# Optimization experiments

Measured on AMD Instinct MI355X. Metric: run time of the kernel, lower is better.

The kernel has to match this reference:

```python
import jax, jax.numpy as jnp
import numpy as np

N_NODES = 8192
N_EDGES = 262144
IN_DIM = 128
HID = 256


def _sage_conv(x, src, dst, w_l, b_l, w_r, n):
    # PyG SAGEConv: out = lin_l(mean_{j in N(i)} x_j) + lin_r(x_i)
    agg = jax.ops.segment_sum(x[src], dst, num_segments=n)          # [n, d]
    deg = jax.ops.segment_sum(jnp.ones_like(src, dtype=x.dtype), dst, num_segments=n)
    mean = agg / jnp.maximum(deg, 1.0)[:, None]
    return mean @ w_l.T + b_l + x @ w_r.T


def setup_inputs() -> dict:
    key = jax.random.key(0)
    ks = jax.random.split(key, 12)
    s = lambda d: 1.0 / np.sqrt(d)
    x = jax.random.normal(ks[0], (N_NODES, IN_DIM), dtype=jnp.float32)
    edge_index = jax.random.randint(ks[1], (2, N_EDGES), 0, N_NODES, dtype=jnp.int64)
    return {
        "x": x,
        "edge_index": edge_index,
        "wl1": jax.random.uniform(ks[2], (HID, IN_DIM), jnp.float32, -s(IN_DIM), s(IN_DIM)),
        "bl1": jax.random.uniform(ks[3], (HID,), jnp.float32, -s(IN_DIM), s(IN_DIM)),
        "wr1": jax.random.uniform(ks[4], (HID, IN_DIM), jnp.float32, -s(IN_DIM), s(IN_DIM)),
        "wl2": jax.random.uniform(ks[5], (HID, HID), jnp.float32, -s(HID), s(HID)),
        "bl2": jax.random.uniform(ks[6], (HID,), jnp.float32, -s(HID), s(HID)),
        "wr2": jax.random.uniform(ks[7], (HID, HID), jnp.float32, -s(HID), s(HID)),
        "w_out": jax.random.uniform(ks[8], (HID, HID), jnp.float32, -s(HID), s(HID)),
        "b_out": jax.random.uniform(ks[9], (HID,), jnp.float32, -s(HID), s(HID)),
        "w_edge": jax.random.uniform(ks[10], (1, 2 * HID), jnp.float32, -s(2 * HID), s(2 * HID)),
        "b_edge": jax.random.uniform(ks[11], (1,), jnp.float32, -s(2 * HID), s(2 * HID)),
    }


def reference(x, edge_index, wl1, bl1, wr1, wl2, bl2, wr2, w_out, b_out, w_edge, b_edge):
    n = x.shape[0]
    src, dst = edge_index[0], edge_index[1]
    h = jax.nn.relu(_sage_conv(x, src, dst, wl1, bl1, wr1, n))
    h = jax.nn.relu(_sage_conv(h, src, dst, wl2, bl2, wr2, n))
    h = h @ w_out.T + b_out                                          # [n, HID]
    # edge_logits[i, j] = edge_proj(cat(h_i, h_j)) == <w_left, h_i> + <w_right, h_j> + b
    w_left, w_right = w_edge[0, :HID], w_edge[0, HID:]
    li = h @ w_left                                                  # [n]
    lj = h @ w_right                                                 # [n]
    return li[:, None] + lj[None, :] + b_edge[0]                     # [n, n]
```

## Files before the change

kernel.cpp:

```cpp
#include <hip/hip_runtime.h>

#define NN   8192
#define NE   262144
#define IND  128
#define HIDD 256

typedef __bf16 v8bf __attribute__((ext_vector_type(8)));
typedef float  v4f  __attribute__((ext_vector_type(4)));

__device__ __forceinline__ float bf2f(unsigned short u) {
  unsigned int v = ((unsigned int)u) << 16;
  return __builtin_bit_cast(float, v);
}
__device__ __forceinline__ unsigned short f2bf(float f) {
  unsigned int u = __builtin_bit_cast(unsigned int, f);
  u += 0x7FFF + ((u >> 16) & 1);
  return (unsigned short)(u >> 16);
}

__global__ void k_prep(const float* __restrict__ wl1, const float* __restrict__ wr1,
                       const float* __restrict__ wl2, const float* __restrict__ wr2,
                       const float* __restrict__ x,
                       const float* __restrict__ w_out, const float* __restrict__ b_out,
                       const float* __restrict__ w_edge,
                       unsigned short* __restrict__ W1, unsigned short* __restrict__ W2,
                       unsigned short* __restrict__ A1,
                       float* __restrict__ VL, float* __restrict__ VR,
                       float* __restrict__ C2,
                       int* __restrict__ CNT,
                       float* __restrict__ LI, float* __restrict__ LJ) {
  __shared__ float red[256];
  int b = blockIdx.x, tid = threadIdx.x;
  if (b < 256) {
    int t = b * 256 + tid;
    int n = t >> 8, k = t & 255;
    float v = (k < 128) ? wl1[n * 128 + k] : wr1[n * 128 + (k - 128)];
    W1[t] = f2bf(v);
  } else if (b < 768) {
    int t = (b - 256) * 256 + tid;
    int n = t >> 9, k = t & 511;
    float v = (k < 256) ? wl2[n * 256 + k] : wr2[n * 256 + (k - 256)];
    W2[t] = f2bf(v);
  } else if (b < 1280) {
    int t = (b - 768) * 256 + tid;
    int row = t >> 4, c8 = (t & 15) << 3;
    const float* xp = &x[row * 128 + c8];
    float4 a = *(const float4*)xp;
    float4 bb = *(const float4*)(xp + 4);
    unsigned short o[8];
    o[0] = f2bf(a.x);  o[1] = f2bf(a.y);  o[2] = f2bf(a.z);  o[3] = f2bf(a.w);
    o[4] = f2bf(bb.x); o[5] = f2bf(bb.y); o[6] = f2bf(bb.z); o[7] = f2bf(bb.w);
    *(uint4*)&A1[row * 256 + 128 + c8] = *(uint4*)o;
  } else if (b < 1312) {
    CNT[(b - 1280) * 256 + tid] = 0;
  } else if (b < 1344) {
    int t = (b - 1312) * 256 + tid;
    LI[t] = 0.f; LJ[t] = 0.f;
  } else {
    int k = tid;
    float al = 0.f, ar = 0.f;
    for (int n = 0; n < 256; n += 8) {
#pragma unroll
      for (int u = 0; u < 8; u++) {
        float w = w_out[(n + u) * 256 + k];
        al = fmaf(w, w_edge[n + u], al);
        ar = fmaf(w, w_edge[256 + n + u], ar);
      }
    }
    VL[k] = al; VR[k] = ar;
    red[k] = b_out[k] * w_edge[k];
    __syncthreads();
    for (int s = 128; s > 0; s >>= 1) { if (k < s) red[k] += red[k + s]; __syncthreads(); }
    if (k == 0) C2[0] = red[0];
    __syncthreads();
    red[k] = b_out[k] * w_edge[256 + k];
    __syncthreads();
    for (int s = 128; s > 0; s >>= 1) { if (k < s) red[k] += red[k + s]; __syncthreads(); }
    if (k == 0) C2[1] = red[0];
  }
}

__global__ void k_count(const int* __restrict__ dst, int* __restrict__ counts) {
  int e = blockIdx.x * 256 + threadIdx.x;
  if (e < NE) atomicAdd(&counts[dst[e]], 1);
}
__global__ void k_scan(const int* __restrict__ counts, int* __restrict__ offs,
                       int* __restrict__ curs, float* __restrict__ ideg) {
  __shared__ int sums[256];
  int t = threadIdx.x;
  int base = t * 32;
  int c[32];
#pragma unroll
  for (int i = 0; i < 32; i += 4) *(int4*)&c[i] = *(const int4*)&counts[base + i];
  int s = 0;
#pragma unroll
  for (int i = 0; i < 32; i++) s += c[i];
  sums[t] = s;
  __syncthreads();
  for (int off = 1; off < 256; off <<= 1) {
    int v = (t >= off) ? sums[t - off] : 0;
    __syncthreads();
    sums[t] += v;
    __syncthreads();
  }
  int run = (t == 0) ? 0 : sums[t - 1];
#pragma unroll
  for (int i = 0; i < 32; i++) {
    offs[base + i] = run;
    curs[base + i] = run;
    ideg[base + i] = 1.0f / (float)(c[i] > 0 ? c[i] : 1);
    run += c[i];
  }
}
__global__ void k_fill(const int* __restrict__ src, const int* __restrict__ dst,
                       int* __restrict__ curs, int* __restrict__ csr) {
  int e = blockIdx.x * 256 + threadIdx.x;
  if (e < NE) {
    int d = dst[e];
    int p = atomicAdd(&curs[d], 1);
    csr[p] = src[e];
  }
}

__global__ void k_gather1(const float* __restrict__ x, unsigned short* __restrict__ A1,
                          const int* __restrict__ offs, const int* __restrict__ counts,
                          const float* __restrict__ ideg, const int* __restrict__ csr) {
  int lane = threadIdx.x & 63;
  int node = blockIdx.x * 4 + (threadIdx.x >> 6);
  int start = offs[node], cnt = counts[node];
  const float2* fp = (const float2*)x + lane;
  float ax0 = 0.f, ay0 = 0.f, ax1 = 0.f, ay1 = 0.f;
  int i = 0;
  for (; i + 8 <= cnt; i += 8) {
    int s0 = csr[start + i + 0], s1 = csr[start + i + 1];
    int s2 = csr[start + i + 2], s3 = csr[start + i + 3];
    int s4 = csr[start + i + 4], s5 = csr[start + i + 5];
    int s6 = csr[start + i + 6], s7 = csr[start + i + 7];
    float2 v0 = fp[(size_t)s0 * 64], v1 = fp[(size_t)s1 * 64];
    float2 v2 = fp[(size_t)s2 * 64], v3 = fp[(size_t)s3 * 64];
    float2 v4 = fp[(size_t)s4 * 64], v5 = fp[(size_t)s5 * 64];
    float2 v6 = fp[(size_t)s6 * 64], v7 = fp[(size_t)s7 * 64];
    ax0 += v0.x; ay0 += v0.y; ax0 += v1.x; ay0 += v1.y;
    ax0 += v2.x; ay0 += v2.y; ax0 += v3.x; ay0 += v3.y;
    ax1 += v4.x; ay1 += v4.y; ax1 += v5.x; ay1 += v5.y;
    ax1 += v6.x; ay1 += v6.y; ax1 += v7.x; ay1 += v7.y;
  }
  for (; i < cnt; i++) {
    float2 v = fp[(size_t)csr[start + i] * 64];
    ax0 += v.x; ay0 += v.y;
  }
  float sc = ideg[node];
  float mx = (ax0 + ax1) * sc, my = (ay0 + ay1) * sc;
  unsigned int o = (unsigned int)f2bf(mx) | ((unsigned int)f2bf(my) << 16);
  *(unsigned int*)&A1[(size_t)node * 256 + lane * 2] = o;
}

__global__ void k_gather2(const unsigned short* __restrict__ A2,
                          unsigned short* __restrict__ A2w,
                          const int* __restrict__ offs, const int* __restrict__ counts,
                          const float* __restrict__ ideg, const int* __restrict__ csr) {
  int lane = threadIdx.x & 63;
  int node = blockIdx.x * 4 + (threadIdx.x >> 6);
  int start = offs[node], cnt = counts[node];
  const unsigned short* fp = A2 + 256 + lane * 4;
  float a0 = 0.f, a1 = 0.f, a2 = 0.f, a3 = 0.f;
#define ACC4(v) { a0 += bf2f((unsigned short)((v).x));        \
                  a1 += bf2f((unsigned short)((v).x >> 16));  \
                  a2 += bf2f((unsigned short)((v).y));        \
                  a3 += bf2f((unsigned short)((v).y >> 16)); }
  int i = 0;
  for (; i + 4 <= cnt; i += 4) {
    int s0 = csr[start + i + 0], s1 = csr[start + i + 1];
    int s2 = csr[start + i + 2], s3 = csr[start + i + 3];
    uint2 v0 = *(const uint2*)&fp[(size_t)s0 * 512];
    uint2 v1 = *(const uint2*)&fp[(size_t)s1 * 512];
    uint2 v2 = *(const uint2*)&fp[(size_t)s2 * 512];
    uint2 v3 = *(const uint2*)&fp[(size_t)s3 * 512];
    ACC4(v0); ACC4(v1); ACC4(v2); ACC4(v3);
  }
  for (; i < cnt; i++) {
    uint2 v = *(const uint2*)&fp[(size_t)csr[start + i] * 512];
    ACC4(v);
  }
#undef ACC4
  float sc = ideg[node];
  unsigned int lo = (unsigned int)f2bf(a0 * sc) | ((unsigned int)f2bf(a1 * sc) << 16);
  unsigned int hi = (unsigned int)f2bf(a2 * sc) | ((unsigned int)f2bf(a3 * sc) << 16);
  uint2 o; o.x = lo; o.y = hi;
  *(uint2*)&A2w[(size_t)node * 512 + lane * 4] = o;
}

__global__ __launch_bounds__(256) void k_gemm(
    const unsigned short* __restrict__ A, int lda,
    const unsigned short* __restrict__ B,
    const float* __restrict__ bias,
    unsigned short* __restrict__ C, int ldc, int coff, int K) {
  __shared__ __align__(16) unsigned short As[64][40];
  __shared__ __align__(16) unsigned short Bs[64][40];
  int tid = threadIdx.x;
  int bm = blockIdx.x, bn = blockIdx.y;
  int lane = tid & 63, wave = tid >> 6;
  int wm = (wave & 1) * 32, wn = (wave >> 1) * 32;
  int quad = lane >> 4, l16 = lane & 15;
  int srow = tid >> 2, schunk = (tid & 3) * 8;
  const unsigned short* gA = A + (size_t)(bm * 64 + srow) * lda + schunk;
  const unsigned short* gB = B + (size_t)(bn * 64 + srow) * K + schunk;
  v4f acc[2][2];
  for (int mi = 0; mi < 2; mi++)
    for (int ni = 0; ni < 2; ni++)
      acc[mi][ni] = v4f{0.f, 0.f, 0.f, 0.f};
  for (int k0 = 0; k0 < K; k0 += 32) {
    uint4 va = *(const uint4*)(gA + k0);
    uint4 vb = *(const uint4*)(gB + k0);
    __syncthreads();
    *(uint4*)&As[srow][schunk] = va;
    *(uint4*)&Bs[srow][schunk] = vb;
    __syncthreads();
    v8bf a0 = *(v8bf*)&As[wm + l16][quad * 8];
    v8bf a1 = *(v8bf*)&As[wm + 16 + l16][quad * 8];
    v8bf b0 = *(v8bf*)&Bs[wn + l16][quad * 8];
    v8bf b1 = *(v8bf*)&Bs[wn + 16 + l16][quad * 8];
    acc[0][0] = __builtin_amdgcn_mfma_f32_16x16x32_bf16(a0, b0, acc[0][0], 0, 0, 0);
    acc[0][1] = __builtin_amdgcn_mfma_f32_16x16x32_bf16(a0, b1, acc[0][1], 0, 0, 0);
    acc[1][0] = __builtin_amdgcn_mfma_f32_16x16x32_bf16(a1, b0, acc[1][0], 0, 0, 0);
    acc[1][1] = __builtin_amdgcn_mfma_f32_16x16x32_bf16(a1, b1, acc[1][1], 0, 0, 0);
  }
  for (int mi = 0; mi < 2; mi++) {
    for (int ni = 0; ni < 2; ni++) {
      int col = bn * 64 + wn + ni * 16 + l16;
      float bv = bias[col];
      for (int r = 0; r < 4; r++) {
        int row = bm * 64 + wm + mi * 16 + quad * 4 + r;
        float v = acc[mi][ni][r] + bv;
        v = fmaxf(v, 0.f);
        C[(size_t)row * ldc + coff + col] = f2bf(v);
      }
    }
  }
}

__global__ __launch_bounds__(256) void k_gemm2_lilj(
    const unsigned short* __restrict__ A,
    const unsigned short* __restrict__ B,
    const float* __restrict__ bias,
    const float* __restrict__ VL, const float* __restrict__ VR,
    float* __restrict__ LI, float* __restrict__ LJ) {
  __shared__ __align__(16) unsigned short As[64][40];
  __shared__ __align__(16) unsigned short Bs[64][40];
  int tid = threadIdx.x;
  int bm = blockIdx.x, bn = blockIdx.y;
  int lane = tid & 63, wave = tid >> 6;
  int wm = (wave & 1) * 32, wn = (wave >> 1) * 32;
  int quad = lane >> 4, l16 = lane & 15;
  int srow = tid >> 2, schunk = (tid & 3) * 8;
  const unsigned short* gA = A + (size_t)(bm * 64 + srow) * 512 + schunk;
  const unsigned short* gB = B + (size_t)(bn * 64 + srow) * 512 + schunk;
  v4f acc[2][2];
  for (int mi = 0; mi < 2; mi++)
    for (int ni = 0; ni < 2; ni++)
      acc[mi][ni] = v4f{0.f, 0.f, 0.f, 0.f};
  for (int k0 = 0; k0 < 512; k0 += 32) {
    uint4 va = *(const uint4*)(gA + k0);
    uint4 vb = *(const uint4*)(gB + k0);
    __syncthreads();
    *(uint4*)&As[srow][schunk] = va;
    *(uint4*)&Bs[srow][schunk] = vb;
    __syncthreads();
    v8bf a0 = *(v8bf*)&As[wm + l16][quad * 8];
    v8bf a1 = *(v8bf*)&As[wm + 16 + l16][quad * 8];
    v8bf b0 = *(v8bf*)&Bs[wn + l16][quad * 8];
    v8bf b1 = *(v8bf*)&Bs[wn + 16 + l16][quad * 8];
    acc[0][0] = __builtin_amdgcn_mfma_f32_16x16x32_bf16(a0, b0, acc[0][0], 0, 0, 0);
    acc[0][1] = __builtin_amdgcn_mfma_f32_16x16x32_bf16(a0, b1, acc[0][1], 0, 0, 0);
    acc[1][0] = __builtin_amdgcn_mfma_f32_16x16x32_bf16(a1, b0, acc[1][0], 0, 0, 0);
    acc[1][1] = __builtin_amdgcn_mfma_f32_16x16x32_bf16(a1, b1, acc[1][1], 0, 0, 0);
  }
  int colb = bn * 64 + wn + l16;
  float vl0 = VL[colb], vl1 = VL[colb + 16];
  float vr0 = VR[colb], vr1 = VR[colb + 16];
  float bv0 = bias[colb], bv1 = bias[colb + 16];
  float pli[8], plj[8];
#pragma unroll
  for (int mi = 0; mi < 2; mi++) {
#pragma unroll
    for (int r = 0; r < 4; r++) {
      float v0 = fmaxf(acc[mi][0][r] + bv0, 0.f);
      float v1 = fmaxf(acc[mi][1][r] + bv1, 0.f);
      pli[mi * 4 + r] = v0 * vl0 + v1 * vl1;
      plj[mi * 4 + r] = v0 * vr0 + v1 * vr1;
    }
  }
#pragma unroll
  for (int off = 1; off < 16; off <<= 1) {
#pragma unroll
    for (int idx = 0; idx < 8; idx++) {
      pli[idx] += __shfl_xor(pli[idx], off);
      plj[idx] += __shfl_xor(plj[idx], off);
    }
  }
  if (l16 == 0) {
#pragma unroll
    for (int mi = 0; mi < 2; mi++) {
#pragma unroll
      for (int r = 0; r < 4; r++) {
        int row = bm * 64 + wm + mi * 16 + quad * 4 + r;
        atomicAdd(&LI[row], pli[mi * 4 + r]);
        atomicAdd(&LJ[row], plj[mi * 4 + r]);
      }
    }
  }
}

__global__ void k_outer(const float* __restrict__ Li, const float* __restrict__ Lj,
                        const float* __restrict__ C2, const float* __restrict__ b_edge,
                        float* __restrict__ outp) {
  int t = blockIdx.x * 256 + threadIdx.x;
  int row = t >> 10;
  int jc = (t & 1023) << 3;
  float cst = C2[0] + C2[1] + b_edge[0];
  float li = Li[row] + cst;
  v4f x0 = *(const v4f*)&Lj[jc];
  v4f x1 = *(const v4f*)&Lj[jc + 4];
  v4f o0 = x0 + li;
  v4f o1 = x1 + li;
  float* op = &outp[(size_t)row * 8192 + jc];
  __builtin_nontemporal_store(o0, (v4f*)op);
  __builtin_nontemporal_store(o1, (v4f*)(op + 4));
}

extern "C" void kernel_launch(void* const* d_in, const int* in_sizes, int n_in,
                              void* d_out, int out_size, void* d_ws, size_t ws_size,
                              hipStream_t stream) {
  const float* x      = (const float*)d_in[0];
  const int*   ei     = (const int*)d_in[1];
  const float* wl1    = (const float*)d_in[2];
  const float* bl1    = (const float*)d_in[3];
  const float* wr1    = (const float*)d_in[4];
  const float* wl2    = (const float*)d_in[5];
  const float* bl2    = (const float*)d_in[6];
  const float* wr2    = (const float*)d_in[7];
  const float* w_out  = (const float*)d_in[8];
  const float* b_out  = (const float*)d_in[9];
  const float* w_edge = (const float*)d_in[10];
  const float* b_edge = (const float*)d_in[11];
  float* outp = (float*)d_out;

  const int* srcp = ei;
  const int* dstp = ei + NE;

  const size_t OFF_A1   = 0;
  const size_t OFF_A2   = OFF_A1 + 4194304;
  const size_t OFF_W1   = OFF_A2 + 8388608;
  const size_t OFF_W2   = OFF_W1 + 131072;
  const size_t OFF_VL   = OFF_W2 + 262144;
  const size_t OFF_VR   = OFF_VL + 1024;
  const size_t OFF_C2   = OFF_VR + 1024;
  const size_t OFF_CNT  = OFF_C2 + 256;
  const size_t OFF_OFFS = OFF_CNT + 32768;
  const size_t OFF_CURS = OFF_OFFS + 32768;
  const size_t OFF_IDEG = OFF_CURS + 32768;
  const size_t OFF_CSR  = OFF_IDEG + 32768;
  const size_t OFF_LI   = OFF_CSR + 1048576;
  const size_t OFF_LJ   = OFF_LI + 32768;
  const size_t TOTAL    = OFF_LJ + 32768;
  if (ws_size < TOTAL) return;

  char* ws = (char*)d_ws;
  unsigned short* A1 = (unsigned short*)(ws + OFF_A1);
  unsigned short* A2 = (unsigned short*)(ws + OFF_A2);
  unsigned short* W1 = (unsigned short*)(ws + OFF_W1);
  unsigned short* W2 = (unsigned short*)(ws + OFF_W2);
  float* VL   = (float*)(ws + OFF_VL);
  float* VR   = (float*)(ws + OFF_VR);
  float* C2   = (float*)(ws + OFF_C2);
  int*   CNT  = (int*)(ws + OFF_CNT);
  int*   OFFS = (int*)(ws + OFF_OFFS);
  int*   CURS = (int*)(ws + OFF_CURS);
  float* IDEG = (float*)(ws + OFF_IDEG);
  int*   CSR  = (int*)(ws + OFF_CSR);
  float* LI   = (float*)(ws + OFF_LI);
  float* LJ   = (float*)(ws + OFF_LJ);

  k_prep<<<1345, 256, 0, stream>>>(wl1, wr1, wl2, wr2, x, w_out, b_out, w_edge,
                                   W1, W2, A1, VL, VR, C2, CNT, LI, LJ);

  k_count<<<NE / 256, 256, 0, stream>>>(dstp, CNT);
  k_scan<<<1, 256, 0, stream>>>(CNT, OFFS, CURS, IDEG);
  k_fill<<<NE / 256, 256, 0, stream>>>(srcp, dstp, CURS, CSR);

  k_gather1<<<NN / 4, 256, 0, stream>>>(x, A1, OFFS, CNT, IDEG, CSR);
  k_gemm<<<dim3(NN / 64, 4), 256, 0, stream>>>(A1, 256, W1, bl1, A2, 512, 256, 256);

  k_gather2<<<NN / 4, 256, 0, stream>>>(A2, A2, OFFS, CNT, IDEG, CSR);
  k_gemm2_lilj<<<dim3(NN / 64, 4), 256, 0, stream>>>(A2, W2, bl2, VL, VR, LI, LJ);

  k_outer<<<(NN * 1024) / 256, 256, 0, stream>>>(LI, LJ, C2, b_edge, outp);
}
```

Before: 454.3 us.

## Simplify gathers to one node per block, scalar per-thread loads, plain stores

Replaces the wave-per-node vectorized gather kernels with simpler kernels that assign one block per node and one scalar feature element per thread. The output kernel swaps its nontemporal vector stores for ordinary float4 stores. This drops the vector loads (float2 and uint2) and the deeper unrolling, and launches far more, smaller blocks. It looks like a simplification or baseline that likely raises gather cost and may pollute the cache on the large output write.

```diff
diff --git a/kernel.cpp b/kernel.cpp
--- a/kernel.cpp
+++ b/kernel.cpp
@@ -122,72 +122,48 @@
   }
 }
 
-__global__ void k_gather1(const float* __restrict__ x, unsigned short* __restrict__ A1,
-                          const int* __restrict__ offs, const int* __restrict__ counts,
-                          const float* __restrict__ ideg, const int* __restrict__ csr) {
-  int lane = threadIdx.x & 63;
-  int node = blockIdx.x * 4 + (threadIdx.x >> 6);
+__global__ void k_gather_f32(const float* __restrict__ feat,
+                             unsigned short* __restrict__ outp,
+                             const int* __restrict__ offs, const int* __restrict__ counts,
+                             const float* __restrict__ ideg, const int* __restrict__ csr) {
+  int node = blockIdx.x;
+  int t = threadIdx.x;
   int start = offs[node], cnt = counts[node];
-  const float2* fp = (const float2*)x + lane;
-  float ax0 = 0.f, ay0 = 0.f, ax1 = 0.f, ay1 = 0.f;
-  int i = 0;
-  for (; i + 8 <= cnt; i += 8) {
-    int s0 = csr[start + i + 0], s1 = csr[start + i + 1];
-    int s2 = csr[start + i + 2], s3 = csr[start + i + 3];
-    int s4 = csr[start + i + 4], s5 = csr[start + i + 5];
-    int s6 = csr[start + i + 6], s7 = csr[start + i + 7];
-    float2 v0 = fp[(size_t)s0 * 64], v1 = fp[(size_t)s1 * 64];
-    float2 v2 = fp[(size_t)s2 * 64], v3 = fp[(size_t)s3 * 64];
-    float2 v4 = fp[(size_t)s4 * 64], v5 = fp[(size_t)s5 * 64];
-    float2 v6 = fp[(size_t)s6 * 64], v7 = fp[(size_t)s7 * 64];
-    ax0 += v0.x; ay0 += v0.y; ax0 += v1.x; ay0 += v1.y;
-    ax0 += v2.x; ay0 += v2.y; ax0 += v3.x; ay0 += v3.y;
-    ax1 += v4.x; ay1 += v4.y; ax1 += v5.x; ay1 += v5.y;
-    ax1 += v6.x; ay1 += v6.y; ax1 += v7.x; ay1 += v7.y;
-  }
-  for (; i < cnt; i++) {
-    float2 v = fp[(size_t)csr[start + i] * 64];
-    ax0 += v.x; ay0 += v.y;
-  }
-  float sc = ideg[node];
-  float mx = (ax0 + ax1) * sc, my = (ay0 + ay1) * sc;
-  unsigned int o = (unsigned int)f2bf(mx) | ((unsigned int)f2bf(my) << 16);
-  *(unsigned int*)&A1[(size_t)node * 256 + lane * 2] = o;
-}
-
-__global__ void k_gather2(const unsigned short* __restrict__ A2,
-                          unsigned short* __restrict__ A2w,
-                          const int* __restrict__ offs, const int* __restrict__ counts,
-                          const float* __restrict__ ideg, const int* __restrict__ csr) {
-  int lane = threadIdx.x & 63;
-  int node = blockIdx.x * 4 + (threadIdx.x >> 6);
-  int start = offs[node], cnt = counts[node];
-  const unsigned short* fp = A2 + 256 + lane * 4;
-  float a0 = 0.f, a1 = 0.f, a2 = 0.f, a3 = 0.f;
-#define ACC4(v) { a0 += bf2f((unsigned short)((v).x));        \
-                  a1 += bf2f((unsigned short)((v).x >> 16));  \
-                  a2 += bf2f((unsigned short)((v).y));        \
-                  a3 += bf2f((unsigned short)((v).y >> 16)); }
+  const float* fp = feat + t;
+  float acc = 0.f;
   int i = 0;
   for (; i + 4 <= cnt; i += 4) {
-    int s0 = csr[start + i + 0], s1 = csr[start + i + 1];
+    int s0 = csr[start + i], s1 = csr[start + i + 1];
     int s2 = csr[start + i + 2], s3 = csr[start + i + 3];
-    uint2 v0 = *(const uint2*)&fp[(size_t)s0 * 512];
-    uint2 v1 = *(const uint2*)&fp[(size_t)s1 * 512];
-    uint2 v2 = *(const uint2*)&fp[(size_t)s2 * 512];
-    uint2 v3 = *(const uint2*)&fp[(size_t)s3 * 512];
-    ACC4(v0); ACC4(v1); ACC4(v2); ACC4(v3);
-  }
-  for (; i < cnt; i++) {
-    uint2 v = *(const uint2*)&fp[(size_t)csr[start + i] * 512];
-    ACC4(v);
-  }
-#undef ACC4
-  float sc = ideg[node];
-  unsigned int lo = (unsigned int)f2bf(a0 * sc) | ((unsigned int)f2bf(a1 * sc) << 16);
-  unsigned int hi = (unsigned int)f2bf(a2 * sc) | ((unsigned int)f2bf(a3 * sc) << 16);
-  uint2 o; o.x = lo; o.y = hi;
-  *(uint2*)&A2w[(size_t)node * 512 + lane * 4] = o;
+    acc += fp[(size_t)s0 * IND];
+    acc += fp[(size_t)s1 * IND];
+    acc += fp[(size_t)s2 * IND];
+    acc += fp[(size_t)s3 * IND];
+  }
+  for (; i < cnt; i++) acc += fp[(size_t)csr[start + i] * IND];
+  outp[(size_t)node * 256 + t] = f2bf(acc * ideg[node]);
+}
+
+__global__ void k_gather_bf16(const unsigned short* __restrict__ feat, int fstride, int foff,
+                              unsigned short* __restrict__ outp, int ostride, int ooff,
+                              const int* __restrict__ offs, const int* __restrict__ counts,
+                              const float* __restrict__ ideg, const int* __restrict__ csr) {
+  int node = blockIdx.x;
+  int t = threadIdx.x;
+  int start = offs[node], cnt = counts[node];
+  const unsigned short* fp = feat + foff + t;
+  float acc = 0.f;
+  int i = 0;
+  for (; i + 4 <= cnt; i += 4) {
+    int s0 = csr[start + i], s1 = csr[start + i + 1];
+    int s2 = csr[start + i + 2], s3 = csr[start + i + 3];
+    acc += bf2f(fp[(size_t)s0 * fstride]);
+    acc += bf2f(fp[(size_t)s1 * fstride]);
+    acc += bf2f(fp[(size_t)s2 * fstride]);
+    acc += bf2f(fp[(size_t)s3 * fstride]);
+  }
+  for (; i < cnt; i++) acc += bf2f(fp[(size_t)csr[start + i] * fstride]);
+  outp[(size_t)node * ostride + ooff + t] = f2bf(acc * ideg[node]);
 }
 
 __global__ __launch_bounds__(256) void k_gemm(
@@ -319,13 +295,14 @@
   int jc = (t & 1023) << 3;
   float cst = C2[0] + C2[1] + b_edge[0];
   float li = Li[row] + cst;
-  v4f x0 = *(const v4f*)&Lj[jc];
-  v4f x1 = *(const v4f*)&Lj[jc + 4];
-  v4f o0 = x0 + li;
-  v4f o1 = x1 + li;
+  float4 x0 = *(const float4*)&Lj[jc];
+  float4 x1 = *(const float4*)&Lj[jc + 4];
+  float4 o0, o1;
+  o0.x = li + x0.x; o0.y = li + x0.y; o0.z = li + x0.z; o0.w = li + x0.w;
+  o1.x = li + x1.x; o1.y = li + x1.y; o1.z = li + x1.z; o1.w = li + x1.w;
   float* op = &outp[(size_t)row * 8192 + jc];
-  __builtin_nontemporal_store(o0, (v4f*)op);
-  __builtin_nontemporal_store(o1, (v4f*)(op + 4));
+  *(float4*)op = o0;
+  *(float4*)(op + 4) = o1;
 }
 
 extern "C" void kernel_launch(void* const* d_in, const int* in_sizes, int n_in,
@@ -388,10 +365,10 @@
   k_scan<<<1, 256, 0, stream>>>(CNT, OFFS, CURS, IDEG);
   k_fill<<<NE / 256, 256, 0, stream>>>(srcp, dstp, CURS, CSR);
 
-  k_gather1<<<NN / 4, 256, 0, stream>>>(x, A1, OFFS, CNT, IDEG, CSR);
+  k_gather_f32<<<NN, 128, 0, stream>>>(x, A1, OFFS, CNT, IDEG, CSR);
   k_gemm<<<dim3(NN / 64, 4), 256, 0, stream>>>(A1, 256, W1, bl1, A2, 512, 256, 256);
 
-  k_gather2<<<NN / 4, 256, 0, stream>>>(A2, A2, OFFS, CNT, IDEG, CSR);
+  k_gather_bf16<<<NN, 256, 0, stream>>>(A2, 512, 256, A2, 512, 0, OFFS, CNT, IDEG, CSR);
   k_gemm2_lilj<<<dim3(NN / 64, 4), 256, 0, stream>>>(A2, W2, bl2, VL, VR, LI, LJ);
 
   k_outer<<<(NN * 1024) / 256, 256, 0, stream>>>(LI, LJ, C2, b_edge, outp);
```

Result: faster. 402.7 us (-11.4%).
